# Kernel optimization log

Hardware: AMD Instinct MI355X
Metric: run time of the kernel (lower is better)

Reference implementation:

```python
import jax, jax.numpy as jnp
import numpy as np

T = 0.2  # temperature

def setup_inputs() -> dict:
    key = jax.random.key(0)
    k1, k2 = jax.random.split(key)
    l_enc = jax.random.normal(k1, (1024, 128, 256), dtype=jnp.float32)
    g_enc = jax.random.normal(k2, (1024, 256), dtype=jnp.float32)
    return {"l_enc": l_enc, "g_enc": g_enc}

def reference(l_enc, g_enc):
    num_assign = l_enc.shape[1]
    l2 = l_enc.reshape(-1, l_enc.shape[-1])           # [N, C], N = B*num_assign
    x_abs = jnp.linalg.norm(l2, axis=1)               # [N]
    g_abs = jnp.linalg.norm(g_enc, axis=1)            # [K]
    # positive pairs: each local row vs its own graph embedding
    g_expand = jnp.repeat(g_enc, num_assign, axis=0)  # [N, C]
    g_expand_abs = jnp.repeat(g_abs, num_assign)      # [N]
    l_pos = jnp.einsum('nc,nc->n', l2, g_expand) / (x_abs * g_expand_abs)
    l_pos = jnp.exp(l_pos / T)                        # [N]
    # full similarity: cosine sim of every local row vs every graph embedding
    sim = jnp.einsum('nc,kc->nk', l2, g_enc) / (x_abs[:, None] * g_abs[None, :])
    sim = jnp.exp(sim / T)                            # [N, K]
    loss = l_pos / (sim.sum(axis=1) - l_pos)
    return -jnp.mean(jnp.log(loss))
```

## Files before the change

kernel.cpp:

```cpp
#include <hip/hip_runtime.h>
#include <hip/hip_bf16.h>
#include <stdint.h>

typedef __bf16 bf16x8 __attribute__((ext_vector_type(8)));
typedef float  f32x16 __attribute__((ext_vector_type(16)));

#define K2EXP 7.2134752044448170f
#define LN2F  0.6931471805599453f

__device__ __forceinline__ unsigned short f2bf(float f) {
  __bf16 h = (__bf16)f;
  return __builtin_bit_cast(unsigned short, h);
}

__global__ __launch_bounds__(256) void k_ghat(const float* __restrict__ g,
                                              char* __restrict__ ghat) {
  const int w = threadIdx.x >> 6, l = threadIdx.x & 63;
  const int row = blockIdx.x * 4 + w;
  const float4 v = *(const float4*)(g + (size_t)row * 256 + l * 4);
  float s = v.x * v.x + v.y * v.y + v.z * v.z + v.w * v.w;
  #pragma unroll
  for (int m = 1; m <= 32; m <<= 1) s += __shfl_xor(s, m, 64);
  const float rn = rsqrtf(s);
  ushort4 o;
  o.x = f2bf(v.x * rn); o.y = f2bf(v.y * rn);
  o.z = f2bf(v.z * rn); o.w = f2bf(v.w * rn);
  const int off = row * 512 + ((l * 8) ^ ((row & 31) << 4));
  *(ushort4*)(ghat + off) = o;
}

__global__ __launch_bounds__(256)
__attribute__((amdgpu_waves_per_eu(2)))
void k_main(const float* __restrict__ l2,
            const char* __restrict__ ghat,
            float* __restrict__ out) {
  __shared__ __align__(16) char smem[2 * 16384 + 512 + 64];
  float* posl = (float*)(smem + 32768);
  float* bsum = (float*)(smem + 32768 + 512);

  const int tid = threadIdx.x;
  const int w   = tid >> 6;
  const int l   = tid & 63;
  const int lm  = l & 31;
  const int lh  = l >> 5;
  const int wrb = blockIdx.x * 128 + w * 32;
  const int p   = blockIdx.x;
  const int pc  = p >> 5;

  if (tid == 0) *bsum = 0.f;

  auto stage = [&](int c, int buf) {
    const char* gsrc = ghat + c * 16384 + tid * 16;
    char* ldst = smem + buf * 16384 + w * 1024;
    #pragma unroll
    for (int i = 0; i < 4; ++i) {
      __builtin_amdgcn_global_load_lds(
          (const __attribute__((address_space(1))) void*)(gsrc + i * 4096),
          (__attribute__((address_space(3))) void*)(ldst + i * 4096),
          16, 0, 0);
    }
  };

  stage(0, 0);

  bf16x8 af0, af1, af2, af3, af4, af5, af6, af7,
         af8, af9, af10, af11, af12, af13, af14, af15;
  float ssq = 0.f;
  const float* rp = l2 + (size_t)(wrb + lm) * 256 + lh * 8;

#define LOADA(s) { \
    const float4 a = *(const float4*)(rp + (s) * 16); \
    const float4 b = *(const float4*)(rp + (s) * 16 + 4); \
    ssq += a.x*a.x + a.y*a.y + a.z*a.z + a.w*a.w \
         + b.x*b.x + b.y*b.y + b.z*b.z + b.w*b.w; \
    bf16x8 f; \
    f[0] = (__bf16)a.x; f[1] = (__bf16)a.y; f[2] = (__bf16)a.z; f[3] = (__bf16)a.w; \
    f[4] = (__bf16)b.x; f[5] = (__bf16)b.y; f[6] = (__bf16)b.z; f[7] = (__bf16)b.w; \
    af##s = f; }

  LOADA(0) LOADA(1) LOADA(2) LOADA(3)
  __builtin_amdgcn_sched_barrier(0);
  LOADA(4) LOADA(5) LOADA(6) LOADA(7)
  __builtin_amdgcn_sched_barrier(0);
  LOADA(8) LOADA(9) LOADA(10) LOADA(11)
  __builtin_amdgcn_sched_barrier(0);
  LOADA(12) LOADA(13) LOADA(14) LOADA(15)
#undef LOADA

  const float rn = rsqrtf(ssq + __shfl_xor(ssq, 32, 64));
#define NRM(s) { bf16x8 f = af##s; \
    f[0] = (__bf16)((float)f[0] * rn); f[1] = (__bf16)((float)f[1] * rn); \
    f[2] = (__bf16)((float)f[2] * rn); f[3] = (__bf16)((float)f[3] * rn); \
    f[4] = (__bf16)((float)f[4] * rn); f[5] = (__bf16)((float)f[5] * rn); \
    f[6] = (__bf16)((float)f[6] * rn); f[7] = (__bf16)((float)f[7] * rn); \
    af##s = f; }
  NRM(0) NRM(1) NRM(2) NRM(3) NRM(4) NRM(5) NRM(6) NRM(7)
  NRM(8) NRM(9) NRM(10) NRM(11) NRM(12) NRM(13) NRM(14) NRM(15)
#undef NRM

  float rs0 = 0.f, rs1 = 0.f, rs2 = 0.f, rs3 = 0.f,
        rs4 = 0.f, rs5 = 0.f, rs6 = 0.f, rs7 = 0.f,
        rs8 = 0.f, rs9 = 0.f, rs10 = 0.f, rs11 = 0.f,
        rs12 = 0.f, rs13 = 0.f, rs14 = 0.f, rs15 = 0.f;

  __syncthreads();

#define MSTEP(s) { \
    const uint4 raw = *(const uint4*)(base + lm * 512 + (((s) * 32 + lh * 16) ^ sw)); \
    acc = __builtin_amdgcn_mfma_f32_32x32x16_bf16( \
              af##s, __builtin_bit_cast(bf16x8, raw), acc, 0, 0, 0); }
#define ESTEP(j) rs##j += __builtin_amdgcn_exp2f(acc[j] * K2EXP);

  const int sw = lm << 4;
  for (int c = 0; c < 32; ++c) {
    if (c < 31) stage(c + 1, (c + 1) & 1);
    const char* base = smem + (c & 1) * 16384;
    f32x16 acc = {0.f};
    MSTEP(0)  MSTEP(1)  MSTEP(2)  MSTEP(3)
    MSTEP(4)  MSTEP(5)  MSTEP(6)  MSTEP(7)
    MSTEP(8)  MSTEP(9)  MSTEP(10) MSTEP(11)
    MSTEP(12) MSTEP(13) MSTEP(14) MSTEP(15)
    ESTEP(0)  ESTEP(1)  ESTEP(2)  ESTEP(3)
    ESTEP(4)  ESTEP(5)  ESTEP(6)  ESTEP(7)
    ESTEP(8)  ESTEP(9)  ESTEP(10) ESTEP(11)
    ESTEP(12) ESTEP(13) ESTEP(14) ESTEP(15)
    if (c == pc && lm == (p & 31)) {
      #pragma unroll
      for (int j = 0; j < 16; ++j) {
        const int r0 = (j & 3) + 8 * (j >> 2) + 4 * lh;
        posl[w * 32 + r0] = acc[j] * K2EXP;
      }
    }
    __syncthreads();
  }
#undef MSTEP
#undef ESTEP

#define RED(j) { float v = rs##j; \
    v += __shfl_xor(v, 1, 64); v += __shfl_xor(v, 2, 64); \
    v += __shfl_xor(v, 4, 64); v += __shfl_xor(v, 8, 64); \
    v += __shfl_xor(v, 16, 64); rs##j = v; }
  RED(0) RED(1) RED(2) RED(3) RED(4) RED(5) RED(6) RED(7)
  RED(8) RED(9) RED(10) RED(11) RED(12) RED(13) RED(14) RED(15)
#undef RED

  if (lm == 0) {
    float local = 0.f;
#define FIN(j) { \
    const int r0 = ((j) & 3) + 8 * ((j) >> 2) + 4 * lh; \
    const float cs = posl[w * 32 + r0]; \
    const float S  = rs##j - __builtin_amdgcn_exp2f(cs); \
    local += (__builtin_amdgcn_logf(S) - cs) * LN2F; }
    FIN(0) FIN(1) FIN(2) FIN(3) FIN(4) FIN(5) FIN(6) FIN(7)
    FIN(8) FIN(9) FIN(10) FIN(11) FIN(12) FIN(13) FIN(14) FIN(15)
#undef FIN
    atomicAdd(bsum, local);
  }
  __syncthreads();
  if (tid == 0) atomicAdd(out, *bsum * (1.0f / 131072.0f));
}

extern "C" void kernel_launch(void* const* d_in, const int* in_sizes, int n_in,
                              void* d_out, int out_size, void* d_ws, size_t ws_size,
                              hipStream_t stream) {
  (void)in_sizes; (void)n_in; (void)out_size; (void)ws_size;
  const float* l2 = (const float*)d_in[0];
  const float* g  = (const float*)d_in[1];
  float* out = (float*)d_out;

  char* ghat = (char*)d_ws;

  hipMemsetAsync(d_out, 0, sizeof(float), stream);
  k_ghat<<<256, 256, 0, stream>>>(g, ghat);
  k_main<<<1024, 256, 0, stream>>>(l2, ghat, out);
}
```

Before: 102.9 us.

## Read B fragments directly from global in MFMA-ready layout, drop LDS staging

The normalized graph embeddings are rewritten into a k-slice-major layout so each lane's MFMA B fragment is one contiguous 16-byte global load. The main kernel drops the double-buffered LDS staging and the per-chunk __syncthreads, reading B straight from global/L2. A sched_barrier splits the MFMA chain. This removes barrier and LDS traffic but relies on L2/L1 caching of the 512KB table shared by all blocks, and exposes global load latency in the MFMA loop.

```diff
diff --git a/kernel.cpp b/kernel.cpp
--- a/kernel.cpp
+++ b/kernel.cpp
@@ -14,7 +14,7 @@
 }
 
 __global__ __launch_bounds__(256) void k_ghat(const float* __restrict__ g,
-                                              char* __restrict__ ghat) {
+                                              char* __restrict__ gt) {
   const int w = threadIdx.x >> 6, l = threadIdx.x & 63;
   const int row = blockIdx.x * 4 + w;
   const float4 v = *(const float4*)(g + (size_t)row * 256 + l * 4);
@@ -25,18 +25,23 @@
   ushort4 o;
   o.x = f2bf(v.x * rn); o.y = f2bf(v.y * rn);
   o.z = f2bf(v.z * rn); o.w = f2bf(v.w * rn);
-  const int off = row * 512 + ((l * 8) ^ ((row & 31) << 4));
-  *(ushort4*)(ghat + off) = o;
+  const unsigned long long pk = __builtin_bit_cast(unsigned long long, o);
+  const unsigned long long lo = __shfl(pk, (l & 31) * 2, 64);
+  const unsigned long long hi = __shfl(pk, (l & 31) * 2 + 1, 64);
+  if (l < 32) {
+    char* dst = gt + (l >> 1) * 32768 + row * 32 + (l & 1) * 16;
+    ((unsigned long long*)dst)[0] = lo;
+    ((unsigned long long*)dst)[1] = hi;
+  }
 }
 
 __global__ __launch_bounds__(256)
 __attribute__((amdgpu_waves_per_eu(2)))
 void k_main(const float* __restrict__ l2,
-            const char* __restrict__ ghat,
+            const char* __restrict__ gt,
             float* __restrict__ out) {
-  __shared__ __align__(16) char smem[2 * 16384 + 512 + 64];
-  float* posl = (float*)(smem + 32768);
-  float* bsum = (float*)(smem + 32768 + 512);
+  __shared__ float posl[128];
+  __shared__ float bsum;
 
   const int tid = threadIdx.x;
   const int w   = tid >> 6;
@@ -45,23 +50,10 @@
   const int lh  = l >> 5;
   const int wrb = blockIdx.x * 128 + w * 32;
   const int p   = blockIdx.x;
-  const int pc  = p >> 5;
+  const int pcf = p >> 5;
+  const int plm = p & 31;
 
-  if (tid == 0) *bsum = 0.f;
-
-  auto stage = [&](int c, int buf) {
-    const char* gsrc = ghat + c * 16384 + tid * 16;
-    char* ldst = smem + buf * 16384 + w * 1024;
-    #pragma unroll
-    for (int i = 0; i < 4; ++i) {
-      __builtin_amdgcn_global_load_lds(
-          (const __attribute__((address_space(1))) void*)(gsrc + i * 4096),
-          (__attribute__((address_space(3))) void*)(ldst + i * 4096),
-          16, 0, 0);
-    }
-  };
-
-  stage(0, 0);
+  if (tid == 0) bsum = 0.f;
 
   bf16x8 af0, af1, af2, af3, af4, af5, af6, af7,
          af8, af9, af10, af11, af12, af13, af14, af15;
@@ -106,32 +98,30 @@
   __syncthreads();
 
 #define MSTEP(s) { \
-    const uint4 raw = *(const uint4*)(base + lm * 512 + (((s) * 32 + lh * 16) ^ sw)); \
+    const uint4 raw = *(const uint4*)(bp + (s) * 32768); \
     acc = __builtin_amdgcn_mfma_f32_32x32x16_bf16( \
               af##s, __builtin_bit_cast(bf16x8, raw), acc, 0, 0, 0); }
 #define ESTEP(j) rs##j += __builtin_amdgcn_exp2f(acc[j] * K2EXP);
 
-  const int sw = lm << 4;
-  for (int c = 0; c < 32; ++c) {
-    if (c < 31) stage(c + 1, (c + 1) & 1);
-    const char* base = smem + (c & 1) * 16384;
+  for (int cf = 0; cf < 32; ++cf) {
+    const char* bp = gt + (size_t)((cf * 32 + lm) * 32 + lh * 16);
     f32x16 acc = {0.f};
     MSTEP(0)  MSTEP(1)  MSTEP(2)  MSTEP(3)
     MSTEP(4)  MSTEP(5)  MSTEP(6)  MSTEP(7)
+    __builtin_amdgcn_sched_barrier(0);
     MSTEP(8)  MSTEP(9)  MSTEP(10) MSTEP(11)
     MSTEP(12) MSTEP(13) MSTEP(14) MSTEP(15)
     ESTEP(0)  ESTEP(1)  ESTEP(2)  ESTEP(3)
     ESTEP(4)  ESTEP(5)  ESTEP(6)  ESTEP(7)
     ESTEP(8)  ESTEP(9)  ESTEP(10) ESTEP(11)
     ESTEP(12) ESTEP(13) ESTEP(14) ESTEP(15)
-    if (c == pc && lm == (p & 31)) {
+    if (cf == pcf && lm == plm) {
       #pragma unroll
       for (int j = 0; j < 16; ++j) {
         const int r0 = (j & 3) + 8 * (j >> 2) + 4 * lh;
         posl[w * 32 + r0] = acc[j] * K2EXP;
       }
     }
-    __syncthreads();
   }
 #undef MSTEP
 #undef ESTEP
@@ -154,10 +144,10 @@
     FIN(0) FIN(1) FIN(2) FIN(3) FIN(4) FIN(5) FIN(6) FIN(7)
     FIN(8) FIN(9) FIN(10) FIN(11) FIN(12) FIN(13) FIN(14) FIN(15)
 #undef FIN
-    atomicAdd(bsum, local);
+    atomicAdd(&bsum, local);
   }
   __syncthreads();
-  if (tid == 0) atomicAdd(out, *bsum * (1.0f / 131072.0f));
+  if (tid == 0) atomicAdd(out, bsum * (1.0f / 131072.0f));
 }
 
 extern "C" void kernel_launch(void* const* d_in, const int* in_sizes, int n_in,
@@ -168,9 +158,9 @@
   const float* g  = (const float*)d_in[1];
   float* out = (float*)d_out;
 
-  char* ghat = (char*)d_ws;
+  char* gt = (char*)d_ws;
 
   hipMemsetAsync(d_out, 0, sizeof(float), stream);
-  k_ghat<<<256, 256, 0, stream>>>(g, ghat);
-  k_main<<<1024, 256, 0, stream>>>(l2, ghat, out);
+  k_ghat<<<256, 256, 0, stream>>>(g, gt);
+  k_main<<<1024, 256, 0, stream>>>(l2, gt, out);
 }
```

Result: slower. 176.5 us (+71.6%).

## Swap MFMA operands so rows land in lanes, cutting row-sum registers and reductions

Applied to the files above, without the earlier changes.

Swaps the MFMA A/B operands so that each lane's accumulator holds the similarities of a single local row. The 16 per-row exp sums therefore collapse into 4 partial accumulators, and the final step needs one cross-half shuffle instead of 16 five-step butterfly reductions. The positive logit is now taken from registers and moved by shuffle, which removes the shared-memory posl buffer. Together with lower register pressure, waves_per_eu is raised from 2 to 3 to allow more occupancy, at the risk of register spills.

```diff
diff --git a/kernel.cpp b/kernel.cpp
--- a/kernel.cpp
+++ b/kernel.cpp
@@ -30,13 +30,12 @@
 }
 
 __global__ __launch_bounds__(256)
-__attribute__((amdgpu_waves_per_eu(2)))
+__attribute__((amdgpu_waves_per_eu(3)))
 void k_main(const float* __restrict__ l2,
             const char* __restrict__ ghat,
             float* __restrict__ out) {
-  __shared__ __align__(16) char smem[2 * 16384 + 512 + 64];
-  float* posl = (float*)(smem + 32768);
-  float* bsum = (float*)(smem + 32768 + 512);
+  __shared__ __align__(16) char smem[2 * 16384 + 64];
+  __shared__ float bsum;
 
   const int tid = threadIdx.x;
   const int w   = tid >> 6;
@@ -46,8 +45,11 @@
   const int wrb = blockIdx.x * 128 + w * 32;
   const int p   = blockIdx.x;
   const int pc  = p >> 5;
+  const int pr  = p & 31;
+  const int lh_p = (pr >> 2) & 1;
+  const int j_p  = (pr & 3) | ((pr >> 3) << 2);
 
-  if (tid == 0) *bsum = 0.f;
+  if (tid == 0) bsum = 0.f;
 
   auto stage = [&](int c, int buf) {
     const char* gsrc = ghat + c * 16384 + tid * 16;
@@ -98,18 +100,15 @@
   NRM(8) NRM(9) NRM(10) NRM(11) NRM(12) NRM(13) NRM(14) NRM(15)
 #undef NRM
 
-  float rs0 = 0.f, rs1 = 0.f, rs2 = 0.f, rs3 = 0.f,
-        rs4 = 0.f, rs5 = 0.f, rs6 = 0.f, rs7 = 0.f,
-        rs8 = 0.f, rs9 = 0.f, rs10 = 0.f, rs11 = 0.f,
-        rs12 = 0.f, rs13 = 0.f, rs14 = 0.f, rs15 = 0.f;
+  float rsa = 0.f, rsb = 0.f, rsc = 0.f, rsd = 0.f;
+  float cs = 0.f;
 
   __syncthreads();
 
 #define MSTEP(s) { \
     const uint4 raw = *(const uint4*)(base + lm * 512 + (((s) * 32 + lh * 16) ^ sw)); \
     acc = __builtin_amdgcn_mfma_f32_32x32x16_bf16( \
-              af##s, __builtin_bit_cast(bf16x8, raw), acc, 0, 0, 0); }
-#define ESTEP(j) rs##j += __builtin_amdgcn_exp2f(acc[j] * K2EXP);
+              __builtin_bit_cast(bf16x8, raw), af##s, acc, 0, 0, 0); }
 
   const int sw = lm << 4;
   for (int c = 0; c < 32; ++c) {
@@ -120,44 +119,42 @@
     MSTEP(4)  MSTEP(5)  MSTEP(6)  MSTEP(7)
     MSTEP(8)  MSTEP(9)  MSTEP(10) MSTEP(11)
     MSTEP(12) MSTEP(13) MSTEP(14) MSTEP(15)
-    ESTEP(0)  ESTEP(1)  ESTEP(2)  ESTEP(3)
-    ESTEP(4)  ESTEP(5)  ESTEP(6)  ESTEP(7)
-    ESTEP(8)  ESTEP(9)  ESTEP(10) ESTEP(11)
-    ESTEP(12) ESTEP(13) ESTEP(14) ESTEP(15)
-    if (c == pc && lm == (p & 31)) {
+    rsa += __builtin_amdgcn_exp2f(acc[0] * K2EXP);
+    rsb += __builtin_amdgcn_exp2f(acc[1] * K2EXP);
+    rsc += __builtin_amdgcn_exp2f(acc[2] * K2EXP);
+    rsd += __builtin_amdgcn_exp2f(acc[3] * K2EXP);
+    rsa += __builtin_amdgcn_exp2f(acc[4] * K2EXP);
+    rsb += __builtin_amdgcn_exp2f(acc[5] * K2EXP);
+    rsc += __builtin_amdgcn_exp2f(acc[6] * K2EXP);
+    rsd += __builtin_amdgcn_exp2f(acc[7] * K2EXP);
+    rsa += __builtin_amdgcn_exp2f(acc[8] * K2EXP);
+    rsb += __builtin_amdgcn_exp2f(acc[9] * K2EXP);
+    rsc += __builtin_amdgcn_exp2f(acc[10] * K2EXP);
+    rsd += __builtin_amdgcn_exp2f(acc[11] * K2EXP);
+    rsa += __builtin_amdgcn_exp2f(acc[12] * K2EXP);
+    rsb += __builtin_amdgcn_exp2f(acc[13] * K2EXP);
+    rsc += __builtin_amdgcn_exp2f(acc[14] * K2EXP);
+    rsd += __builtin_amdgcn_exp2f(acc[15] * K2EXP);
+    if (c == pc) {
       #pragma unroll
-      for (int j = 0; j < 16; ++j) {
-        const int r0 = (j & 3) + 8 * (j >> 2) + 4 * lh;
-        posl[w * 32 + r0] = acc[j] * K2EXP;
-      }
+      for (int j = 0; j < 16; ++j)
+        if (j == j_p && lh == lh_p) cs = acc[j] * K2EXP;
     }
     __syncthreads();
   }
 #undef MSTEP
-#undef ESTEP
 
-#define RED(j) { float v = rs##j; \
-    v += __shfl_xor(v, 1, 64); v += __shfl_xor(v, 2, 64); \
-    v += __shfl_xor(v, 4, 64); v += __shfl_xor(v, 8, 64); \
-    v += __shfl_xor(v, 16, 64); rs##j = v; }
-  RED(0) RED(1) RED(2) RED(3) RED(4) RED(5) RED(6) RED(7)
-  RED(8) RED(9) RED(10) RED(11) RED(12) RED(13) RED(14) RED(15)
-#undef RED
-
-  if (lm == 0) {
-    float local = 0.f;
-#define FIN(j) { \
-    const int r0 = ((j) & 3) + 8 * ((j) >> 2) + 4 * lh; \
-    const float cs = posl[w * 32 + r0]; \
-    const float S  = rs##j - __builtin_amdgcn_exp2f(cs); \
-    local += (__builtin_amdgcn_logf(S) - cs) * LN2F; }
-    FIN(0) FIN(1) FIN(2) FIN(3) FIN(4) FIN(5) FIN(6) FIN(7)
-    FIN(8) FIN(9) FIN(10) FIN(11) FIN(12) FIN(13) FIN(14) FIN(15)
-#undef FIN
-    atomicAdd(bsum, local);
-  }
+  float rs = (rsa + rsb) + (rsc + rsd);
+  rs += __shfl_xor(rs, 32, 64);
+  cs = __shfl(cs, lm | (lh_p << 5), 64);
+  const float S = rs - __builtin_amdgcn_exp2f(cs);
+  float term = (__builtin_amdgcn_logf(S) - cs) * LN2F;
+  term += __shfl_xor(term, 1, 64);  term += __shfl_xor(term, 2, 64);
+  term += __shfl_xor(term, 4, 64);  term += __shfl_xor(term, 8, 64);
+  term += __shfl_xor(term, 16, 64);
+  if (l == 0) atomicAdd(&bsum, term);
   __syncthreads();
-  if (tid == 0) atomicAdd(out, *bsum * (1.0f / 131072.0f));
+  if (tid == 0) atomicAdd(out, bsum * (1.0f / 131072.0f));
 }
 
 extern "C" void kernel_launch(void* const* d_in, const int* in_sizes, int n_in,
```

Measured after the change: 95.65 us. -7.0%, faster.
